# Kernel optimization log

Hardware: AMD Instinct MI355X
Metric: run time of the kernel (lower is better)

Reference implementation:

```python
import jax, jax.numpy as jnp
import numpy as np

N_NODES = 50000
N_EDGES = 800000
N_GRAPHS = 128
IN_CH = 31
HID = 64
EPS = 1e-5


def _glorot(key, shape, scale=0.05):
    return jax.random.normal(key, shape, dtype=jnp.float32) * scale


def setup_inputs() -> dict:
    key = jax.random.key(0)
    ks = jax.random.split(key, 16)
    x = jax.random.normal(ks[0], (N_NODES, IN_CH), dtype=jnp.float32)
    edge_index = jax.random.randint(ks[1], (2, N_EDGES), 0, N_NODES, dtype=jnp.int32)
    batch = jnp.sort(jax.random.randint(ks[2], (N_NODES,), 0, N_GRAPHS, dtype=jnp.int32))
    params = {
        "t": jnp.ones((1,), dtype=jnp.float32),  # shared learnable softmax temperature
        "W1r": _glorot(ks[3], (HID, IN_CH)), "b1": jnp.zeros((HID,), jnp.float32), "W1s": _glorot(ks[4], (HID, IN_CH)),
        "W2r": _glorot(ks[5], (HID, HID)),  "b2": jnp.zeros((HID,), jnp.float32), "W2s": _glorot(ks[6], (HID, HID)),
        "W3r": _glorot(ks[7], (HID, HID)),  "b3": jnp.zeros((HID,), jnp.float32), "W3s": _glorot(ks[8], (HID, HID)),
        "Wl1": _glorot(ks[9], (2 * HID, 3 * HID)), "bl1": jnp.zeros((2 * HID,), jnp.float32),
        "Wl2": _glorot(ks[10], (HID // 2, 2 * HID)), "bl2": jnp.zeros((HID // 2,), jnp.float32),
    }
    return {"x": x, "edge_index": edge_index, "batch": batch, **params}


def _softmax_aggr(m, dst, t, n):
    # segment-softmax over incoming edges, per channel: alpha = softmax(t*m | dst)
    logits = m * t  # [E, C]
    mx = jax.ops.segment_max(logits, dst, num_segments=n)  # [N, C]
    e = jnp.exp(logits - mx[dst])
    denom = jax.ops.segment_sum(e, dst, num_segments=n)
    alpha = e / denom[dst]
    return jax.ops.segment_sum(m * alpha, dst, num_segments=n)  # [N, C]


def _graph_conv(x, src, dst, t, Wr, br, Ws):
    # PyG GraphConv: out = lin_rel(aggr_j x_j) + lin_root(x); lin_root has no bias
    m = x[src]  # gather [E, C]
    aggr = _softmax_aggr(m, dst, t, x.shape[0])
    return aggr @ Wr.T + br + x @ Ws.T


def _instance_norm(x):
    # torch InstanceNorm1d on [N, C] input -> normalize each row over feature dim
    mu = jnp.mean(x, axis=1, keepdims=True)
    var = jnp.mean((x - mu) ** 2, axis=1, keepdims=True)
    return (x - mu) / jnp.sqrt(var + EPS)


def reference(x, edge_index, batch, t, W1r, b1, W1s, W2r, b2, W2s, W3r, b3, W3s, Wl1, bl1, Wl2, bl2):
    src, dst = edge_index[0], edge_index[1]
    x1 = jax.nn.relu(_instance_norm(_graph_conv(x, src, dst, t, W1r, b1, W1s)))
    x2 = jax.nn.relu(_instance_norm(_graph_conv(x1, src, dst, t, W2r, b2, W2s)))
    x3 = jax.nn.relu(_instance_norm(_graph_conv(x2, src, dst, t, W3r, b3, W3s)))
    h1 = jax.ops.segment_max(x1, batch, num_segments=N_GRAPHS)
    h2 = jax.ops.segment_max(x2, batch, num_segments=N_GRAPHS)
    h3 = jax.ops.segment_max(x3, batch, num_segments=N_GRAPHS)
    h = jnp.concatenate([h1, h2, h3], axis=1)  # [G, 3*HID]
    z = jax.nn.relu(h @ Wl1.T + bl1)  # dropout is identity in eval mode
    z = z @ Wl2.T + bl2
    norm = jnp.maximum(jnp.linalg.norm(z, axis=1, keepdims=True), 1e-12)
    return z / norm
```

## Files before the change

kernel.cpp:

```cpp
#include <hip/hip_runtime.h>
#include <hip/hip_fp16.h>

#define N_NODES 50000
#define N_EDGES 800000
#define N_GRAPHS 128
#define IN_CH 31
#define HID 64

typedef __attribute__((ext_vector_type(8))) short short8;
typedef __attribute__((ext_vector_type(8))) unsigned short ushort8;
typedef __attribute__((ext_vector_type(4))) float floatx4;
typedef __attribute__((ext_vector_type(8))) _Float16 half8;

__device__ inline unsigned short f2h(float f) {
    __half h = __float2half_rn(f);
    return __half_as_ushort(h);
}
__device__ inline unsigned packh2(float a, float b) {
    __half2 h = __floats2half2_rn(a, b);
    return *(unsigned*)&h;
}
__device__ inline void pack4h(short* p, float4 v) {
    unsigned lo = packh2(v.x, v.y);
    unsigned hi = packh2(v.z, v.w);
    *(uint2*)p = make_uint2(lo, hi);
}

__global__ void prep_kernel(const float* __restrict__ x,
                            unsigned short* __restrict__ xh32, int nN) {
    int i = blockIdx.x * 256 + threadIdx.x;
    if (i >= nN * 32) return;
    int node = i >> 5, c = i & 31;
    xh32[i] = (c < IN_CH) ? f2h(x[node * IN_CH + c]) : 0;
}


#define BKT_SHIFT 7
#define BKT_MAX 512
#define CHUNK 8192
#define CAP 2560

__global__ void bucket_scatter_kernel(const int* __restrict__ src,
                                      const int* __restrict__ dst,
                                      int* __restrict__ bucket_cnt,
                                      unsigned* __restrict__ ebuf, int e, int nb) {
    __shared__ int bins[BKT_MAX];
    __shared__ int base[BKT_MAX];
    __shared__ int lcur[BKT_MAX];
    int tid = threadIdx.x;
    int i0 = blockIdx.x * CHUNK;
    int i1 = i0 + CHUNK; if (i1 > e) i1 = e;
    for (int k = tid; k < nb; k += 256) { bins[k] = 0; lcur[k] = 0; }
    __syncthreads();
    for (int j = i0 + tid; j < i1; j += 256)
        atomicAdd(&bins[dst[j] >> BKT_SHIFT], 1);
    __syncthreads();
    for (int k = tid; k < nb; k += 256)
        if (bins[k]) base[k] = atomicAdd(&bucket_cnt[k], bins[k]);
    __syncthreads();
    for (int j = i0 + tid; j < i1; j += 256) {
        int ss = src[j], dd = dst[j];
        int b = dd >> BKT_SHIFT;
        int p = atomicAdd(&lcur[b], 1);
        ebuf[(size_t)b * CAP + base[b] + p] = (unsigned)ss | ((unsigned)(dd & 127) << 16);
    }
}

__global__ void bucket_csr_kernel(const unsigned* __restrict__ ebuf,
                                  const int* __restrict__ bucket_cnt,
                                  int* __restrict__ row_ptr, int* __restrict__ deg,
                                  int* __restrict__ csr_src, int nN) {
    __shared__ int nh[128];
    __shared__ int s[128];
    __shared__ int ncur[128];
    int tid = threadIdx.x;
    int b = blockIdx.x;
    int cnt = bucket_cnt[b];
    size_t boff = (size_t)b * CAP;
    int node0 = b << BKT_SHIFT;
    if (tid < 128) nh[tid] = 0;
    __syncthreads();
    for (int j = tid; j < cnt; j += 256)
        atomicAdd(&nh[ebuf[boff + j] >> 16], 1);
    __syncthreads();
    int v = (tid < 128) ? nh[tid] : 0;
    if (tid < 128) s[tid] = v;
    __syncthreads();
    for (int off = 1; off < 128; off <<= 1) {
        int u = (tid < 128 && tid >= off) ? s[tid - off] : 0;
        __syncthreads();
        if (tid < 128) s[tid] += u;
        __syncthreads();
    }
    if (tid < 128 && node0 + tid < nN) {
        int excl = (int)boff + s[tid] - v;
        row_ptr[node0 + tid] = excl;
        deg[node0 + tid] = v;
        ncur[tid] = excl;
    }
    __syncthreads();
    for (int j = tid; j < cnt; j += 256) {
        unsigned ed = ebuf[boff + j];
        int pos = atomicAdd(&ncur[ed >> 16], 1);
        csr_src[pos] = (int)(ed & 0xFFFF);
    }
}


template <int C_IN>
__global__ void __launch_bounds__(256, 8) aggr_kernel(
        const unsigned short* __restrict__ Ytab,
        const float* __restrict__ tptr,
        const int* __restrict__ row_ptr, const int* __restrict__ deg,
        const int* __restrict__ csr_src,
        unsigned short* __restrict__ aRowsB, int n) {
    constexpr int RS = (C_IN == 64) ? 64 : 32;
    int w = threadIdx.x >> 6, l = threadIdx.x & 63;
    int d = blockIdx.x * 4 + w;
    if (d >= n) return;
    int beg = __builtin_amdgcn_readfirstlane(row_ptr[d]);
    int dg  = __builtin_amdgcn_readfirstlane(deg[d]);
    int end = beg + dg;
    int cl = l & (RS - 1);
    float tval = tptr[0];

    float den = 0.f, num = 0.f;
    for (int base = beg; base < end; base += 64) {
        int cend = base + 64; if (cend > end) cend = end;
        int chunk = cend - base;
        int sidx = csr_src[base + ((l < chunk) ? l : 0)];
        for (int j0 = 0; j0 < chunk; j0 += 8) {
            int jc = chunk - j0;
            float yv[8];
            #pragma unroll
            for (int p = 0; p < 8; ++p) {
                int jj = (p < jc) ? (j0 + p) : (chunk - 1);
                int s  = __builtin_amdgcn_readlane(sidx, jj);
                yv[p] = (float)*(const _Float16*)&Ytab[(size_t)s * RS + cl];
            }
            #pragma unroll
            for (int p = 0; p < 8; ++p) {
                float m = (p < jc) ? 1.f : 0.f;
                float E = __expf(tval * yv[p]) * m;
                den += E;
                num = fmaf(yv[p], E, num);
            }
        }
    }
    float aggr = (dg > 0 && den > 0.f) ? num / den : 0.f;

    if constexpr (C_IN == 64) {
        aRowsB[(size_t)d * 64 + l] = f2h(aggr);
    } else {
        unsigned short outv;
        if (l < C_IN)               outv = f2h(aggr);
        else if (l < 2 * C_IN)      outv = Ytab[(size_t)d * 32 + (l - C_IN)];
        else                        outv = 0;
        aRowsB[(size_t)d * 64 + l] = outv;
    }
}


template <int C_IN, bool WY>
__global__ void __launch_bounds__(256, 4) transform_kernel(
        const unsigned short* __restrict__ aRowsB, const unsigned short* __restrict__ yprev,
        const int* __restrict__ batch,
        const float* __restrict__ Wr, const float* __restrict__ br,
        const float* __restrict__ Ws,
        unsigned short* __restrict__ yout,
        float* __restrict__ hmax, int n) {
    constexpr int K_TOT = (C_IN == 64) ? 128 : 64;
    constexpr int KP    = K_TOT + 8;
    constexpr int KS    = K_TOT / 32;
    constexpr int ABSH  = 2 * 64 * KP;
    constexpr int CSH   = 64 * 68 * 2;
    constexpr int SMSH  = (ABSH > CSH) ? ABSH : CSH;

    __shared__ short smem[SMSH];
    short* sA = smem;
    short* sB = smem + 64 * KP;
    float* sC = (float*)smem;

    int tid = threadIdx.x;
    int nb = blockIdx.x * 64;

    if constexpr (C_IN == 64) {
        for (int idx = tid; idx < 64 * 16; idx += 256) {
            int row = idx >> 4, c8 = idx & 15;
            int node = nb + row; if (node >= n) node = n - 1;
            ushort8 v = (c8 < 8) ? ((const ushort8*)(aRowsB + (size_t)node * 64))[c8]
                                 : ((const ushort8*)(yprev + (size_t)node * 64))[c8 - 8];
            *(ushort8*)&sA[row * KP + c8 * 8] = v;
        }
        for (int idx = tid; idx < 64 * 32; idx += 256) {
            int nr = idx >> 5, c4 = idx & 31;
            float4 v = (c4 < 16) ? ((const float4*)(Wr + nr * 64))[c4]
                                 : ((const float4*)(Ws + nr * 64))[c4 - 16];
            pack4h(&sB[nr * KP + c4 * 4], v);
        }
    } else {
        for (int idx = tid; idx < 64 * 8; idx += 256) {
            int row = idx >> 3, c8 = idx & 7;
            int node = nb + row; if (node >= n) node = n - 1;
            ushort8 v = ((const ushort8*)(aRowsB + (size_t)node * 64))[c8];
            *(ushort8*)&sA[row * KP + c8 * 8] = v;
        }
        for (int idx = tid; idx < 64 * 64; idx += 256) {
            int nr = idx >> 6, k = idx & 63;
            float v = (k < C_IN) ? Wr[nr * C_IN + k]
                    : (k < 2 * C_IN) ? Ws[nr * C_IN + (k - C_IN)] : 0.f;
            sB[nr * KP + k] = (short)f2h(v);
        }
    }
    __syncthreads();

    int w = tid >> 6, l = tid & 63;
    int m = l & 15;
    int q = l >> 4;
    floatx4 acc[4] = {{0.f,0.f,0.f,0.f},{0.f,0.f,0.f,0.f},
                      {0.f,0.f,0.f,0.f},{0.f,0.f,0.f,0.f}};
    const short* aBase = &sA[(w * 16 + m) * KP + q * 8];
    #pragma unroll 2
    for (int s = 0; s < KS; ++s) {
        half8 af = *(const half8*)(aBase + s * 32);
        #pragma unroll
        for (int t = 0; t < 4; ++t) {
            half8 bf = *(const half8*)&sB[(t * 16 + m) * KP + q * 8 + s * 32];
            acc[t] = __builtin_amdgcn_mfma_f32_16x16x32_f16(af, bf, acc[t], 0, 0, 0);
        }
    }

    __syncthreads();
    #pragma unroll
    for (int t = 0; t < 4; ++t)
        #pragma unroll
        for (int r = 0; r < 4; ++r)
            sC[(w * 16 + q * 4 + r) * 68 + t * 16 + m] = acc[t][r];
    __syncthreads();

    float bias = br[l];
    int gcur = -1;
    float rmax = 0.f;
    for (int i = 0; i < 16; ++i) {
        int j = w * 16 + i;
        int d = nb + j;
        if (d < n) {
            float a = sC[j * 68 + l] + bias;
            float s = a;
            for (int off = 32; off > 0; off >>= 1) s += __shfl_xor(s, off);
            float mu = s * (1.0f / 64.0f);
            float dc = a - mu;
            float s2 = dc * dc;
            for (int off = 32; off > 0; off >>= 1) s2 += __shfl_xor(s2, off);
            float var = s2 * (1.0f / 64.0f);
            float y = dc * rsqrtf(var + 1e-5f);
            y = fmaxf(y, 0.f);
            if constexpr (WY) {
                yout[(size_t)d * 64 + l] = f2h(y);
            }
            int g = __builtin_amdgcn_readfirstlane(batch[d]);
            if (g != gcur) {
                if (gcur >= 0)
                    atomicMax((int*)&hmax[gcur * 64 + l], __float_as_int(rmax));
                gcur = g;
                rmax = 0.f;
            }
            rmax = fmaxf(rmax, y);
        }
    }
    if (gcur >= 0)
        atomicMax((int*)&hmax[gcur * 64 + l], __float_as_int(rmax));
}


__global__ void mlp_kernel(const float* __restrict__ h,
                           const float* __restrict__ Wl1, const float* __restrict__ bl1,
                           const float* __restrict__ Wl2, const float* __restrict__ bl2,
                           float* __restrict__ out) {
    __shared__ float hrow[192];
    __shared__ float z1[128];
    __shared__ float z2[32];
    __shared__ float snorm;
    int g = blockIdx.x, tid = threadIdx.x;
    if (tid < 64) {
        hrow[tid]       = h[0 * N_GRAPHS * 64 + g * 64 + tid];
        hrow[64 + tid]  = h[1 * N_GRAPHS * 64 + g * 64 + tid];
        hrow[128 + tid] = h[2 * N_GRAPHS * 64 + g * 64 + tid];
    }
    __syncthreads();
    float acc = bl1[tid];
    #pragma unroll 8
    for (int c = 0; c < 192; ++c) acc = fmaf(hrow[c], Wl1[tid * 192 + c], acc);
    z1[tid] = fmaxf(acc, 0.f);
    __syncthreads();
    if (tid < 32) {
        float a2 = bl2[tid];
        #pragma unroll 8
        for (int c = 0; c < 128; ++c) a2 = fmaf(z1[c], Wl2[tid * 128 + c], a2);
        z2[tid] = a2;
    }
    __syncthreads();
    if (tid == 0) {
        float ss = 0.f;
        for (int i = 0; i < 32; ++i) ss += z2[i] * z2[i];
        snorm = fmaxf(sqrtf(ss), 1e-12f);
    }
    __syncthreads();
    if (tid < 32) out[g * 32 + tid] = z2[tid] / snorm;
}


extern "C" void kernel_launch(void* const* d_in, const int* in_sizes, int n_in,
                              void* d_out, int out_size, void* d_ws, size_t ws_size,
                              hipStream_t stream) {
    const float* x   = (const float*)d_in[0];
    const int* eidx  = (const int*)d_in[1];
    const int* batch = (const int*)d_in[2];
    const float* t   = (const float*)d_in[3];
    const float* W1r = (const float*)d_in[4];
    const float* b1  = (const float*)d_in[5];
    const float* W1s = (const float*)d_in[6];
    const float* W2r = (const float*)d_in[7];
    const float* b2  = (const float*)d_in[8];
    const float* W2s = (const float*)d_in[9];
    const float* W3r = (const float*)d_in[10];
    const float* b3  = (const float*)d_in[11];
    const float* W3s = (const float*)d_in[12];
    const float* Wl1 = (const float*)d_in[13];
    const float* bl1 = (const float*)d_in[14];
    const float* Wl2 = (const float*)d_in[15];
    const float* bl2 = (const float*)d_in[16];
    float* out = (float*)d_out;

    const int nE = in_sizes[1] / 2;
    const int nN = in_sizes[2];
    const int* src = eidx;
    const int* dst = eidx + nE;
    const int nb = (nN + 127) >> BKT_SHIFT;

    char* ws = (char*)d_ws;
    size_t off = 0;
    auto alloc = [&](size_t bytes) {
        char* p = ws + off;
        off = (off + bytes + 255) & ~(size_t)255;
        return p;
    };
    int*            bucket_cnt = (int*)alloc((size_t)BKT_MAX * 4);
    float*          h          = (float*)alloc((size_t)3 * N_GRAPHS * 64 * 4);
    int*            row_ptr    = (int*)alloc((size_t)nN * 4);
    int*            deg        = (int*)alloc((size_t)nN * 4);
    unsigned*       ebuf       = (unsigned*)alloc((size_t)nb * CAP * 4);
    int*            csr_src    = (int*)alloc((size_t)nb * CAP * 4);
    unsigned short* xh32       = (unsigned short*)alloc((size_t)nN * 32 * 2);
    unsigned short* yAh        = (unsigned short*)alloc((size_t)nN * 64 * 2);
    unsigned short* yBh        = (unsigned short*)alloc((size_t)nN * 64 * 2);
    unsigned short* aRowsB     = (unsigned short*)alloc((size_t)nN * 64 * 2);

    const int nbChunk = (nE + CHUNK - 1) / CHUNK;

    hipMemsetAsync(bucket_cnt, 0,
                   (char*)(h + 3 * N_GRAPHS * 64) - (char*)bucket_cnt, stream);
    prep_kernel<<<(nN * 32 + 255) / 256, 256, 0, stream>>>(x, xh32, nN);
    bucket_scatter_kernel<<<nbChunk, 256, 0, stream>>>(src, dst, bucket_cnt, ebuf, nE, nb);
    bucket_csr_kernel<<<nb, 256, 0, stream>>>(ebuf, bucket_cnt, row_ptr, deg, csr_src, nN);

    const int nbA = (nN + 3) / 4;
    const int nbT = (nN + 63) / 64;

    aggr_kernel<IN_CH><<<nbA, 256, 0, stream>>>(xh32, t, row_ptr, deg, csr_src, aRowsB, nN);
    transform_kernel<IN_CH, true><<<nbT, 256, 0, stream>>>(
        aRowsB, nullptr, batch, W1r, b1, W1s, yAh, h + 0 * N_GRAPHS * 64, nN);

    aggr_kernel<HID><<<nbA, 256, 0, stream>>>(yAh, t, row_ptr, deg, csr_src, aRowsB, nN);
    transform_kernel<HID, true><<<nbT, 256, 0, stream>>>(
        aRowsB, yAh, batch, W2r, b2, W2s, yBh, h + 1 * N_GRAPHS * 64, nN);

    aggr_kernel<HID><<<nbA, 256, 0, stream>>>(yBh, t, row_ptr, deg, csr_src, aRowsB, nN);
    transform_kernel<HID, false><<<nbT, 256, 0, stream>>>(
        aRowsB, yBh, batch, W3r, b3, W3s, nullptr, h + 2 * N_GRAPHS * 64, nN);

    mlp_kernel<<<N_GRAPHS, 128, 0, stream>>>(h, Wl1, bl1, Wl2, bl2, out);
}
```

Before: 266.6 us.

## Process two destination nodes per wavefront in aggregation and fuse prep into scatter

The aggregation kernel now has each wavefront handle two destination nodes at once. It interleaves their gathers in 16-wide unrolled batches, which raises memory-level parallelism and hides gather latency. Row pointer and degree are packed into one int2 array so each node needs one load. The fp16 conversion of x is folded into the bucket scatter launch as extra blocks, saving a kernel launch. The cost is more registers per thread, which may lower occupancy, and load imbalance when the two paired nodes have different degrees.

```diff
diff --git a/kernel.cpp b/kernel.cpp
--- a/kernel.cpp
+++ b/kernel.cpp
@@ -26,24 +26,27 @@
     *(uint2*)p = make_uint2(lo, hi);
 }
 
-__global__ void prep_kernel(const float* __restrict__ x,
-                            unsigned short* __restrict__ xh32, int nN) {
-    int i = blockIdx.x * 256 + threadIdx.x;
-    if (i >= nN * 32) return;
-    int node = i >> 5, c = i & 31;
-    xh32[i] = (c < IN_CH) ? f2h(x[node * IN_CH + c]) : 0;
-}
-
 
 #define BKT_SHIFT 7
 #define BKT_MAX 512
 #define CHUNK 8192
 #define CAP 2560
 
-__global__ void bucket_scatter_kernel(const int* __restrict__ src,
-                                      const int* __restrict__ dst,
-                                      int* __restrict__ bucket_cnt,
-                                      unsigned* __restrict__ ebuf, int e, int nb) {
+__global__ void scatter_prep_kernel(const int* __restrict__ src,
+                                    const int* __restrict__ dst,
+                                    int* __restrict__ bucket_cnt,
+                                    unsigned* __restrict__ ebuf, int e, int nb,
+                                    int nbChunk,
+                                    const float* __restrict__ x,
+                                    unsigned short* __restrict__ xh32, int nN) {
+    if (blockIdx.x >= nbChunk) {
+        int i = (blockIdx.x - nbChunk) * 256 + threadIdx.x;
+        if (i < nN * 32) {
+            int node = i >> 5, c = i & 31;
+            xh32[i] = (c < IN_CH) ? f2h(x[node * IN_CH + c]) : 0;
+        }
+        return;
+    }
     __shared__ int bins[BKT_MAX];
     __shared__ int base[BKT_MAX];
     __shared__ int lcur[BKT_MAX];
@@ -68,7 +71,7 @@
 
 __global__ void bucket_csr_kernel(const unsigned* __restrict__ ebuf,
                                   const int* __restrict__ bucket_cnt,
-                                  int* __restrict__ row_ptr, int* __restrict__ deg,
+                                  int2* __restrict__ rpdeg,
                                   int* __restrict__ csr_src, int nN) {
     __shared__ int nh[128];
     __shared__ int s[128];
@@ -94,8 +97,7 @@
     }
     if (tid < 128 && node0 + tid < nN) {
         int excl = (int)boff + s[tid] - v;
-        row_ptr[node0 + tid] = excl;
-        deg[node0 + tid] = v;
+        rpdeg[node0 + tid] = make_int2(excl, v);
         ncur[tid] = excl;
     }
     __syncthreads();
@@ -111,52 +113,94 @@
 __global__ void __launch_bounds__(256, 8) aggr_kernel(
         const unsigned short* __restrict__ Ytab,
         const float* __restrict__ tptr,
-        const int* __restrict__ row_ptr, const int* __restrict__ deg,
+        const int2* __restrict__ rpdeg,
         const int* __restrict__ csr_src,
         unsigned short* __restrict__ aRowsB, int n) {
     constexpr int RS = (C_IN == 64) ? 64 : 32;
     int w = threadIdx.x >> 6, l = threadIdx.x & 63;
-    int d = blockIdx.x * 4 + w;
-    if (d >= n) return;
-    int beg = __builtin_amdgcn_readfirstlane(row_ptr[d]);
-    int dg  = __builtin_amdgcn_readfirstlane(deg[d]);
-    int end = beg + dg;
+    int dA = (blockIdx.x * 4 + w) * 2;
+    if (dA >= n) return;
+    int dB = dA + 1;
+    bool hasB = (dB < n);
+    int2 ra = rpdeg[dA];
+    int2 rb = hasB ? rpdeg[dB] : make_int2(0, 0);
+    int begA = __builtin_amdgcn_readfirstlane(ra.x);
+    int dgA  = __builtin_amdgcn_readfirstlane(ra.y);
+    int begB = __builtin_amdgcn_readfirstlane(rb.x);
+    int dgB  = hasB ? __builtin_amdgcn_readfirstlane(rb.y) : 0;
     int cl = l & (RS - 1);
     float tval = tptr[0];
 
-    float den = 0.f, num = 0.f;
-    for (int base = beg; base < end; base += 64) {
-        int cend = base + 64; if (cend > end) cend = end;
-        int chunk = cend - base;
-        int sidx = csr_src[base + ((l < chunk) ? l : 0)];
-        for (int j0 = 0; j0 < chunk; j0 += 8) {
-            int jc = chunk - j0;
-            float yv[8];
-            #pragma unroll
-            for (int p = 0; p < 8; ++p) {
-                int jj = (p < jc) ? (j0 + p) : (chunk - 1);
-                int s  = __builtin_amdgcn_readlane(sidx, jj);
-                yv[p] = (float)*(const _Float16*)&Ytab[(size_t)s * RS + cl];
-            }
-            #pragma unroll
-            for (int p = 0; p < 8; ++p) {
-                float m = (p < jc) ? 1.f : 0.f;
-                float E = __expf(tval * yv[p]) * m;
-                den += E;
-                num = fmaf(yv[p], E, num);
-            }
-        }
-    }
-    float aggr = (dg > 0 && den > 0.f) ? num / den : 0.f;
+    float denA = 0.f, numA = 0.f, denB = 0.f, numB = 0.f;
+    int nckA = (dgA + 63) >> 6, nckB = (dgB + 63) >> 6;
+    int ncl = nckA > nckB ? nckA : nckB;
+    for (int c = 0; c < ncl; ++c) {
+        int chA = dgA - c * 64; chA = chA > 64 ? 64 : chA;
+        int chB = dgB - c * 64; chB = chB > 64 ? 64 : chB;
+        int sidxA = 0, sidxB = 0;
+        if (chA > 0) sidxA = csr_src[begA + c * 64 + ((l < chA) ? l : chA - 1)];
+        if (chB > 0) sidxB = csr_src[begB + c * 64 + ((l < chB) ? l : chB - 1)];
+        int mx = chA > chB ? chA : chB;
+        for (int j0 = 0; j0 < mx; j0 += 16) {
+            int jcA = chA - j0;
+            int jcB = chB - j0;
+            unsigned vA[16], vB[16];
+            if (jcA > 0) {
+                #pragma unroll
+                for (int p = 0; p < 16; ++p) {
+                    int jj = (p < jcA) ? (j0 + p) : (chA - 1);
+                    int s  = __builtin_amdgcn_readlane(sidxA, jj);
+                    vA[p] = Ytab[(size_t)s * RS + cl];
+                }
+            }
+            if (jcB > 0) {
+                #pragma unroll
+                for (int p = 0; p < 16; ++p) {
+                    int jj = (p < jcB) ? (j0 + p) : (chB - 1);
+                    int s  = __builtin_amdgcn_readlane(sidxB, jj);
+                    vB[p] = Ytab[(size_t)s * RS + cl];
+                }
+            }
+            if (jcA > 0) {
+                #pragma unroll
+                for (int p = 0; p < 16; ++p) {
+                    float m  = (p < jcA) ? 1.f : 0.f;
+                    float yv = __half2float(__ushort_as_half((unsigned short)vA[p]));
+                    float E  = __expf(tval * yv) * m;
+                    denA += E;
+                    numA = fmaf(yv, E, numA);
+                }
+            }
+            if (jcB > 0) {
+                #pragma unroll
+                for (int p = 0; p < 16; ++p) {
+                    float m  = (p < jcB) ? 1.f : 0.f;
+                    float yv = __half2float(__ushort_as_half((unsigned short)vB[p]));
+                    float E  = __expf(tval * yv) * m;
+                    denB += E;
+                    numB = fmaf(yv, E, numB);
+                }
+            }
+        }
+    }
+    float aggrA = (dgA > 0 && denA > 0.f) ? numA / denA : 0.f;
+    float aggrB = (dgB > 0 && denB > 0.f) ? numB / denB : 0.f;
 
     if constexpr (C_IN == 64) {
-        aRowsB[(size_t)d * 64 + l] = f2h(aggr);
+        aRowsB[(size_t)dA * 64 + l] = f2h(aggrA);
+        if (hasB) aRowsB[(size_t)dB * 64 + l] = f2h(aggrB);
     } else {
-        unsigned short outv;
-        if (l < C_IN)               outv = f2h(aggr);
-        else if (l < 2 * C_IN)      outv = Ytab[(size_t)d * 32 + (l - C_IN)];
-        else                        outv = 0;
-        aRowsB[(size_t)d * 64 + l] = outv;
+        unsigned short outA, outB;
+        if (l < C_IN)               outA = f2h(aggrA);
+        else if (l < 2 * C_IN)      outA = Ytab[(size_t)dA * 32 + (l - C_IN)];
+        else                        outA = 0;
+        aRowsB[(size_t)dA * 64 + l] = outA;
+        if (hasB) {
+            if (l < C_IN)           outB = f2h(aggrB);
+            else if (l < 2 * C_IN)  outB = Ytab[(size_t)dB * 32 + (l - C_IN)];
+            else                    outB = 0;
+            aRowsB[(size_t)dB * 64 + l] = outB;
+        }
     }
 }
 
@@ -347,8 +391,7 @@
     };
     int*            bucket_cnt = (int*)alloc((size_t)BKT_MAX * 4);
     float*          h          = (float*)alloc((size_t)3 * N_GRAPHS * 64 * 4);
-    int*            row_ptr    = (int*)alloc((size_t)nN * 4);
-    int*            deg        = (int*)alloc((size_t)nN * 4);
+    int2*           rpdeg      = (int2*)alloc((size_t)nN * 8);
     unsigned*       ebuf       = (unsigned*)alloc((size_t)nb * CAP * 4);
     int*            csr_src    = (int*)alloc((size_t)nb * CAP * 4);
     unsigned short* xh32       = (unsigned short*)alloc((size_t)nN * 32 * 2);
@@ -357,25 +400,26 @@
     unsigned short* aRowsB     = (unsigned short*)alloc((size_t)nN * 64 * 2);
 
     const int nbChunk = (nE + CHUNK - 1) / CHUNK;
+    const int prepB   = (nN * 32 + 255) / 256;
 
     hipMemsetAsync(bucket_cnt, 0,
                    (char*)(h + 3 * N_GRAPHS * 64) - (char*)bucket_cnt, stream);
-    prep_kernel<<<(nN * 32 + 255) / 256, 256, 0, stream>>>(x, xh32, nN);
-    bucket_scatter_kernel<<<nbChunk, 256, 0, stream>>>(src, dst, bucket_cnt, ebuf, nE, nb);
-    bucket_csr_kernel<<<nb, 256, 0, stream>>>(ebuf, bucket_cnt, row_ptr, deg, csr_src, nN);
-
-    const int nbA = (nN + 3) / 4;
+    scatter_prep_kernel<<<nbChunk + prepB, 256, 0, stream>>>(
+        src, dst, bucket_cnt, ebuf, nE, nb, nbChunk, x, xh32, nN);
+    bucket_csr_kernel<<<nb, 256, 0, stream>>>(ebuf, bucket_cnt, rpdeg, csr_src, nN);
+
+    const int nbA = (nN + 7) / 8;
     const int nbT = (nN + 63) / 64;
 
-    aggr_kernel<IN_CH><<<nbA, 256, 0, stream>>>(xh32, t, row_ptr, deg, csr_src, aRowsB, nN);
+    aggr_kernel<IN_CH><<<nbA, 256, 0, stream>>>(xh32, t, rpdeg, csr_src, aRowsB, nN);
     transform_kernel<IN_CH, true><<<nbT, 256, 0, stream>>>(
         aRowsB, nullptr, batch, W1r, b1, W1s, yAh, h + 0 * N_GRAPHS * 64, nN);
 
-    aggr_kernel<HID><<<nbA, 256, 0, stream>>>(yAh, t, row_ptr, deg, csr_src, aRowsB, nN);
+    aggr_kernel<HID><<<nbA, 256, 0, stream>>>(yAh, t, rpdeg, csr_src, aRowsB, nN);
     transform_kernel<HID, true><<<nbT, 256, 0, stream>>>(
         aRowsB, yAh, batch, W2r, b2, W2s, yBh, h + 1 * N_GRAPHS * 64, nN);
 
-    aggr_kernel<HID><<<nbA, 256, 0, stream>>>(yBh, t, row_ptr, deg, csr_src, aRowsB, nN);
+    aggr_kernel<HID><<<nbA, 256, 0, stream>>>(yBh, t, rpdeg, csr_src, aRowsB, nN);
     transform_kernel<HID, false><<<nbT, 256, 0, stream>>>(
         aRowsB, yBh, batch, W3r, b3, W3s, nullptr, h + 2 * N_GRAPHS * 64, nN);
 
```

Result: slower. 285.8 us (+7.2%).

## Split hidden features into two 32-channel planes and aggregate each plane separately

Applied to the files above, without the earlier changes.

Stores the layer outputs as two planar halves of 32 fp16 channels (each node row is 64 bytes) instead of interleaved 64-channel rows. Each 64-channel aggregation becomes two passes over 32-channel planes, and each wave processes two edges per load, one per half-wave, then merges the two halves with a shuffle. The aim is a smaller gather working set per pass so it fits better in L2/MALL, and fuller use of the lanes in the 31-channel first layer. In exchange, the CSR index reads and launch overhead double for layers 2 and 3, and the transform kernel's loads and stores now use the planar layout.

```diff
diff --git a/kernel.cpp b/kernel.cpp
--- a/kernel.cpp
+++ b/kernel.cpp
@@ -107,56 +107,62 @@
 }
 
 
-template <int C_IN>
-__global__ void __launch_bounds__(256, 8) aggr_kernel(
-        const unsigned short* __restrict__ Ytab,
+template <bool WITH_X>
+__global__ void __launch_bounds__(256, 8) aggr_pass(
+        const unsigned short* __restrict__ plane,
         const float* __restrict__ tptr,
         const int* __restrict__ row_ptr, const int* __restrict__ deg,
         const int* __restrict__ csr_src,
-        unsigned short* __restrict__ aRowsB, int n) {
-    constexpr int RS = (C_IN == 64) ? 64 : 32;
+        unsigned short* __restrict__ aRowsB, int outOff, int n) {
     int w = threadIdx.x >> 6, l = threadIdx.x & 63;
     int d = blockIdx.x * 4 + w;
     if (d >= n) return;
     int beg = __builtin_amdgcn_readfirstlane(row_ptr[d]);
     int dg  = __builtin_amdgcn_readfirstlane(deg[d]);
     int end = beg + dg;
-    int cl = l & (RS - 1);
+    int cl = l & 31;
+    int half = l >> 5;
     float tval = tptr[0];
 
     float den = 0.f, num = 0.f;
     for (int base = beg; base < end; base += 64) {
         int cend = base + 64; if (cend > end) cend = end;
         int chunk = cend - base;
-        int sidx = csr_src[base + ((l < chunk) ? l : 0)];
-        for (int j0 = 0; j0 < chunk; j0 += 8) {
-            int jc = chunk - j0;
-            float yv[8];
+        int sidx = csr_src[base + ((l < chunk) ? l : chunk - 1)];
+        for (int j0 = 0; j0 < chunk; j0 += 16) {
+            unsigned short v[8];
             #pragma unroll
             for (int p = 0; p < 8; ++p) {
-                int jj = (p < jc) ? (j0 + p) : (chunk - 1);
-                int s  = __builtin_amdgcn_readlane(sidx, jj);
-                yv[p] = (float)*(const _Float16*)&Ytab[(size_t)s * RS + cl];
+                int ja = j0 + 2 * p;     if (ja >= chunk) ja = chunk - 1;
+                int jb = j0 + 2 * p + 1; if (jb >= chunk) jb = chunk - 1;
+                int sa = __builtin_amdgcn_readlane(sidx, ja);
+                int sb = __builtin_amdgcn_readlane(sidx, jb);
+                int s  = half ? sb : sa;
+                v[p] = plane[(size_t)s * 32 + cl];
             }
             #pragma unroll
             for (int p = 0; p < 8; ++p) {
-                float m = (p < jc) ? 1.f : 0.f;
-                float E = __expf(tval * yv[p]) * m;
+                float m  = (j0 + 2 * p + half < chunk) ? 1.f : 0.f;
+                float yv = __half2float(__ushort_as_half(v[p]));
+                float E  = __expf(tval * yv) * m;
                 den += E;
-                num = fmaf(yv[p], E, num);
-            }
-        }
-    }
+                num = fmaf(yv, E, num);
+            }
+        }
+    }
+    num += __shfl_xor(num, 32);
+    den += __shfl_xor(den, 32);
     float aggr = (dg > 0 && den > 0.f) ? num / den : 0.f;
 
-    if constexpr (C_IN == 64) {
-        aRowsB[(size_t)d * 64 + l] = f2h(aggr);
-    } else {
+    if constexpr (WITH_X) {
         unsigned short outv;
-        if (l < C_IN)               outv = f2h(aggr);
-        else if (l < 2 * C_IN)      outv = Ytab[(size_t)d * 32 + (l - C_IN)];
+        if (l < IN_CH)              outv = f2h(aggr);
+        else if (l < 2 * IN_CH)     outv = plane[(size_t)d * 32 + (l - IN_CH)];
         else                        outv = 0;
         aRowsB[(size_t)d * 64 + l] = outv;
+    } else {
+        if (l < 32)
+            aRowsB[(size_t)d * 64 + outOff + l] = f2h(aggr);
     }
 }
 
@@ -188,8 +194,14 @@
         for (int idx = tid; idx < 64 * 16; idx += 256) {
             int row = idx >> 4, c8 = idx & 15;
             int node = nb + row; if (node >= n) node = n - 1;
-            ushort8 v = (c8 < 8) ? ((const ushort8*)(aRowsB + (size_t)node * 64))[c8]
-                                 : ((const ushort8*)(yprev + (size_t)node * 64))[c8 - 8];
+            ushort8 v;
+            if (c8 < 8) {
+                v = ((const ushort8*)(aRowsB + (size_t)node * 64))[c8];
+            } else {
+                int pl = (c8 - 8) >> 2;
+                v = ((const ushort8*)(yprev + (size_t)pl * n * 32
+                                            + (size_t)node * 32))[(c8 - 8) & 3];
+            }
             *(ushort8*)&sA[row * KP + c8 * 8] = v;
         }
         for (int idx = tid; idx < 64 * 32; idx += 256) {
@@ -256,7 +268,7 @@
             float y = dc * rsqrtf(var + 1e-5f);
             y = fmaxf(y, 0.f);
             if constexpr (WY) {
-                yout[(size_t)d * 64 + l] = f2h(y);
+                yout[(size_t)(l >> 5) * n * 32 + (size_t)d * 32 + (l & 31)] = f2h(y);
             }
             int g = __builtin_amdgcn_readfirstlane(batch[d]);
             if (g != gcur) {
@@ -367,15 +379,17 @@
     const int nbA = (nN + 3) / 4;
     const int nbT = (nN + 63) / 64;
 
-    aggr_kernel<IN_CH><<<nbA, 256, 0, stream>>>(xh32, t, row_ptr, deg, csr_src, aRowsB, nN);
+    aggr_pass<true><<<nbA, 256, 0, stream>>>(xh32, t, row_ptr, deg, csr_src, aRowsB, 0, nN);
     transform_kernel<IN_CH, true><<<nbT, 256, 0, stream>>>(
         aRowsB, nullptr, batch, W1r, b1, W1s, yAh, h + 0 * N_GRAPHS * 64, nN);
 
-    aggr_kernel<HID><<<nbA, 256, 0, stream>>>(yAh, t, row_ptr, deg, csr_src, aRowsB, nN);
+    aggr_pass<false><<<nbA, 256, 0, stream>>>(yAh,            t, row_ptr, deg, csr_src, aRowsB, 0,  nN);
+    aggr_pass<false><<<nbA, 256, 0, stream>>>(yAh + (size_t)nN * 32, t, row_ptr, deg, csr_src, aRowsB, 32, nN);
     transform_kernel<HID, true><<<nbT, 256, 0, stream>>>(
         aRowsB, yAh, batch, W2r, b2, W2s, yBh, h + 1 * N_GRAPHS * 64, nN);
 
-    aggr_kernel<HID><<<nbA, 256, 0, stream>>>(yBh, t, row_ptr, deg, csr_src, aRowsB, nN);
+    aggr_pass<false><<<nbA, 256, 0, stream>>>(yBh,            t, row_ptr, deg, csr_src, aRowsB, 0,  nN);
+    aggr_pass<false><<<nbA, 256, 0, stream>>>(yBh + (size_t)nN * 32, t, row_ptr, deg, csr_src, aRowsB, 32, nN);
     transform_kernel<HID, false><<<nbT, 256, 0, stream>>>(
         aRowsB, yBh, batch, W3r, b3, W3s, nullptr, h + 2 * N_GRAPHS * 64, nN);
 
```

New measurement: 319.0 us. 19.7% more time.
